# Optimization experiments

Hardware: AMD Instinct MI355X
Metric: run time of the kernel (lower is better)

Reference implementation:

```python
import jax, jax.numpy as jnp
import numpy as np

B, S, H, D = 2, 2048, 8, 64
W = 128  # attention window radius


def setup_inputs() -> dict:
    key = jax.random.key(0)
    kq, kk, kv = jax.random.split(key, 3)
    return {
        "query": jax.random.normal(kq, (B, S, H, D), dtype=jnp.float32),
        "key": jax.random.normal(kk, (B, S, H, D), dtype=jnp.float32),
        "value": jax.random.normal(kv, (B, S, H, D), dtype=jnp.float32),
        "window_size": W,
    }


def reference(query, key, value, window_size):
    # Sliding-window (symmetric, radius=window_size, inclusive) attention.
    # Per-query softmax over keys j with |i - j| <= window_size, scale 1/sqrt(D).
    b, s, h, d = query.shape
    scale = 1.0 / jnp.sqrt(jnp.asarray(d, query.dtype))
    # scores: [B, H, S, S]
    scores = jnp.einsum("bihd,bjhd->bhij", query * scale, key)
    i = jnp.arange(s)[:, None]
    j = jnp.arange(s)[None, :]
    band = jnp.abs(i - j) <= window_size  # [S, S]
    scores = jnp.where(band, scores, -jnp.inf)
    weights = jax.nn.softmax(scores, axis=-1)
    out = jnp.einsum("bhij,bjhd->bihd", weights, value)
    return out
```

## Files before the change

kernel.cpp:

```cpp
#include <hip/hip_runtime.h>
#include <hip/hip_fp16.h>
#include <math.h>

typedef _Float16 half8 __attribute__((ext_vector_type(8)));
typedef _Float16 half4 __attribute__((ext_vector_type(4)));
typedef float f32x4 __attribute__((ext_vector_type(4)));

#define S_LEN 2048
#define NH 8
#define DH 64
#define HD (NH*DH)
#define BQ 64
#define SPAN 320
#define NT 256

__global__ __launch_bounds__(NT, 2)
void swa_mfma(const float* __restrict__ qg, const float* __restrict__ kg,
              const float* __restrict__ vg, const int* __restrict__ wptr,
              float* __restrict__ outg)
{
    __shared__ __align__(16) unsigned short Kl[SPAN * DH];
    __shared__ __align__(16) unsigned short Vt[DH * SPAN];

    int W = *wptr; if (W > 128) W = 128;
    const int span = BQ + 2 * W;

    const int t = threadIdx.x;
    int bid = blockIdx.x;
    bid = (bid & 7) * (gridDim.x >> 3) + (bid >> 3);
    const int qt = bid & 31, h = (bid >> 5) & 7, b = bid >> 8;
    const int i0 = qt * BQ, s0 = i0 - W;

    const float* kbh = kg + (size_t)b * S_LEN * HD + h * DH;
    const float* vbh = vg + (size_t)b * S_LEN * HD + h * DH;

    for (int cidx = t; cidx < span * 8; cidx += NT) {
        const int koff = cidx >> 3, cr = cidx & 7;
        const int j = s0 + koff;
        const int dst = koff * 64 + ((cr ^ (koff & 7)) << 3);
        half8 hv = {0,0,0,0,0,0,0,0};
        if ((unsigned)j < S_LEN) {
            const float* p = kbh + (size_t)j * HD + cr * 8;
            float4 f0 = *(const float4*)p, f1 = *(const float4*)(p + 4);
            hv[0]=(_Float16)f0.x; hv[1]=(_Float16)f0.y; hv[2]=(_Float16)f0.z; hv[3]=(_Float16)f0.w;
            hv[4]=(_Float16)f1.x; hv[5]=(_Float16)f1.y; hv[6]=(_Float16)f1.z; hv[7]=(_Float16)f1.w;
        }
        *(half8*)(&Kl[dst]) = hv;
    }

    for (int task = t; task < span * 4; task += NT) {
        const int dq = task & 15, kq = task >> 4;
        float rr[4][4];
        #pragma unroll
        for (int jj = 0; jj < 4; ++jj) {
            const int j = s0 + kq * 4 + jj;
            float4 f = {0.f, 0.f, 0.f, 0.f};
            if ((unsigned)j < S_LEN) f = *(const float4*)(vbh + (size_t)j * HD + dq * 4);
            rr[jj][0] = f.x; rr[jj][1] = f.y; rr[jj][2] = f.z; rr[jj][3] = f.w;
        }
        #pragma unroll
        for (int i = 0; i < 4; ++i) {
            const int dim = dq * 4 + i;
            half4 w = { (_Float16)rr[0][i], (_Float16)rr[1][i],
                        (_Float16)rr[2][i], (_Float16)rr[3][i] };
            const int off = dim * SPAN + (((kq >> 1) ^ (dim & 7)) << 3) + ((kq & 1) << 2);
            *(half4*)(&Vt[off]) = w;
        }
    }

    const int wid = t >> 6, lane = t & 63, c = lane & 15, g = lane >> 4;
    const int q = i0 + wid * 16 + c;
    const float* qrow = qg + (size_t)b * S_LEN * HD + h * DH + (size_t)q * HD;
    half8 qa0, qa1;
    #pragma unroll
    for (int e = 0; e < 8; ++e) {
        qa0[e] = (_Float16)(qrow[g * 8 + e] * 0.125f);
        qa1[e] = (_Float16)(qrow[32 + g * 8 + e] * 0.125f);
    }

    const int c7 = c & 7;
    const int ch0 = (g ^ c7) << 3;
    const int ch1 = ((g + 4) ^ c7) << 3;
    int lo = q - W; if (lo < 0) lo = 0;
    int hi = q + W; if (hi > S_LEN - 1) hi = S_LEN - 1;
    const unsigned rng = (unsigned)(hi - lo);

    int ts = wid >> 1;
    const int ts0 = (s0 < 0) ? ((-s0) >> 5) : 0;
    if (ts0 > ts) ts = ts0;
    const int te_w = (16 * wid + 15 + 2 * W) >> 5;
    const int te_s = (S_LEN - 1 - s0) >> 5;
    const int te = te_w < te_s ? te_w : te_s;

    float m = -1e4f, l = 0.f;
    f32x4 o0 = {0,0,0,0}, o1 = {0,0,0,0}, o2 = {0,0,0,0}, o3 = {0,0,0,0};

    __syncthreads();

    for (int t32 = ts; t32 <= te; ++t32) {
        const unsigned short* krow = &Kl[(t32 * 32 + c) * 64];
        half8 k00 = *(const half8*)(krow + ch0);
        half8 k01 = *(const half8*)(krow + ch1);
        half8 k10 = *(const half8*)(krow + 16 * 64 + ch0);
        half8 k11 = *(const half8*)(krow + 16 * 64 + ch1);
        f32x4 st0 = {0,0,0,0}, st1 = {0,0,0,0};
        st0 = __builtin_amdgcn_mfma_f32_16x16x32_f16(k00, qa0, st0, 0, 0, 0);
        st0 = __builtin_amdgcn_mfma_f32_16x16x32_f16(k01, qa1, st0, 0, 0, 0);
        st1 = __builtin_amdgcn_mfma_f32_16x16x32_f16(k10, qa0, st1, 0, 0, 0);
        st1 = __builtin_amdgcn_mfma_f32_16x16x32_f16(k11, qa1, st1, 0, 0, 0);

        const int kb = s0 + t32 * 32 + 4 * g;
        float sv0[4], sv1[4];
        #pragma unroll
        for (int r = 0; r < 4; ++r) {
            sv0[r] = ((unsigned)(kb + r - lo) <= rng)      ? st0[r] : -30000.f;
            sv1[r] = ((unsigned)(kb + 16 + r - lo) <= rng) ? st1[r] : -30000.f;
        }
        float tmax = fmaxf(fmaxf(fmaxf(sv0[0], sv0[1]), fmaxf(sv0[2], sv0[3])),
                           fmaxf(fmaxf(sv1[0], sv1[1]), fmaxf(sv1[2], sv1[3])));
        tmax = fmaxf(tmax, __shfl_xor(tmax, 16));
        tmax = fmaxf(tmax, __shfl_xor(tmax, 32));
        const float newm = fmaxf(m, tmax);
        const float alpha = __expf(m - newm);
        m = newm;
        l *= alpha;
        o0 *= alpha; o1 *= alpha; o2 *= alpha; o3 *= alpha;

        float p0[4], p1[4], ls = 0.f;
        #pragma unroll
        for (int r = 0; r < 4; ++r) {
            p0[r] = __expf(sv0[r] - m);
            p1[r] = __expf(sv1[r] - m);
            ls += p0[r] + p1[r];
        }
        l += ls;
        half8 pb;
        #pragma unroll
        for (int r = 0; r < 4; ++r) { pb[r] = (_Float16)p0[r]; pb[4 + r] = (_Float16)p1[r]; }

        const int cb = 4 * t32 + (g >> 1);
        const int off1 = ((cb ^ c7) << 3) + ((g & 1) << 2);
        const int off2 = (((cb + 2) ^ c7) << 3) + ((g & 1) << 2);
#define PV_STEP(DF, OACC) { \
        const unsigned short* vrow = &Vt[(16 * DF + c) * SPAN]; \
        half4 vlo = *(const half4*)(vrow + off1); \
        half4 vhi = *(const half4*)(vrow + off2); \
        half8 vf; \
        vf[0]=vlo[0]; vf[1]=vlo[1]; vf[2]=vlo[2]; vf[3]=vlo[3]; \
        vf[4]=vhi[0]; vf[5]=vhi[1]; vf[6]=vhi[2]; vf[7]=vhi[3]; \
        OACC = __builtin_amdgcn_mfma_f32_16x16x32_f16(vf, pb, OACC, 0, 0, 0); }
        PV_STEP(0, o0)
        PV_STEP(1, o1)
        PV_STEP(2, o2)
        PV_STEP(3, o3)
#undef PV_STEP
    }

    l += __shfl_xor(l, 16);
    l += __shfl_xor(l, 32);
    const float inv = 1.0f / l;
    float* orow = outg + (size_t)b * S_LEN * HD + h * DH + (size_t)q * HD + 4 * g;
    { float4 w; w.x=o0[0]*inv; w.y=o0[1]*inv; w.z=o0[2]*inv; w.w=o0[3]*inv; *(float4*)(orow)      = w; }
    { float4 w; w.x=o1[0]*inv; w.y=o1[1]*inv; w.z=o1[2]*inv; w.w=o1[3]*inv; *(float4*)(orow + 16) = w; }
    { float4 w; w.x=o2[0]*inv; w.y=o2[1]*inv; w.z=o2[2]*inv; w.w=o2[3]*inv; *(float4*)(orow + 32) = w; }
    { float4 w; w.x=o3[0]*inv; w.y=o3[1]*inv; w.z=o3[2]*inv; w.w=o3[3]*inv; *(float4*)(orow + 48) = w; }
}

extern "C" void kernel_launch(void* const* d_in, const int* in_sizes, int n_in,
                              void* d_out, int out_size, void* d_ws, size_t ws_size,
                              hipStream_t stream) {
    const float* q = (const float*)d_in[0];
    const float* k = (const float*)d_in[1];
    const float* v = (const float*)d_in[2];
    const int*   w = (const int*)d_in[3];
    float* out = (float*)d_out;

    const int nblocks = 2 * NH * (S_LEN / BQ);
    swa_mfma<<<dim3(nblocks), dim3(NT), 0, stream>>>(q, k, v, w, out);
}
```

Baseline: 19.38 us.

## Double-buffer K/V chunks in LDS with register prefetch overlapping MFMA compute

The whole K/V window is no longer staged into LDS up front. The loop now streams 64-key chunks through two LDS buffers, prefetching the next chunk into registers during compute and writing it after. Other changes: log2e is folded into the Q scale so exp2f replaces expf, the rescale is skipped when no lane's max grows, MFMA sections get raised s_setprio, and Q is loaded vectorised. This cuts LDS footprint and start-up latency, at the cost of a __syncthreads per chunk and more live registers.

```diff
diff --git a/kernel.cpp b/kernel.cpp
--- a/kernel.cpp
+++ b/kernel.cpp
@@ -11,19 +11,20 @@
 #define DH 64
 #define HD (NH*DH)
 #define BQ 64
-#define SPAN 320
 #define NT 256
+#define CK 64
 
 __global__ __launch_bounds__(NT, 2)
 void swa_mfma(const float* __restrict__ qg, const float* __restrict__ kg,
               const float* __restrict__ vg, const int* __restrict__ wptr,
               float* __restrict__ outg)
 {
-    __shared__ __align__(16) unsigned short Kl[SPAN * DH];
-    __shared__ __align__(16) unsigned short Vt[DH * SPAN];
+    __shared__ __align__(16) unsigned short Kb[2][CK * DH];
+    __shared__ __align__(16) unsigned short Vb[2][DH * CK];
 
     int W = *wptr; if (W > 128) W = 128;
     const int span = BQ + 2 * W;
+    const int nch = (span + CK - 1) / CK;
 
     const int t = threadIdx.x;
     int bid = blockIdx.x;
@@ -34,48 +35,73 @@
     const float* kbh = kg + (size_t)b * S_LEN * HD + h * DH;
     const float* vbh = vg + (size_t)b * S_LEN * HD + h * DH;
 
-    for (int cidx = t; cidx < span * 8; cidx += NT) {
-        const int koff = cidx >> 3, cr = cidx & 7;
-        const int j = s0 + koff;
-        const int dst = koff * 64 + ((cr ^ (koff & 7)) << 3);
-        half8 hv = {0,0,0,0,0,0,0,0};
-        if ((unsigned)j < S_LEN) {
-            const float* p = kbh + (size_t)j * HD + cr * 8;
-            float4 f0 = *(const float4*)p, f1 = *(const float4*)(p + 4);
-            hv[0]=(_Float16)f0.x; hv[1]=(_Float16)f0.y; hv[2]=(_Float16)f0.z; hv[3]=(_Float16)f0.w;
-            hv[4]=(_Float16)f1.x; hv[5]=(_Float16)f1.y; hv[6]=(_Float16)f1.z; hv[7]=(_Float16)f1.w;
-        }
-        *(half8*)(&Kl[dst]) = hv;
-    }
-
-    for (int task = t; task < span * 4; task += NT) {
-        const int dq = task & 15, kq = task >> 4;
-        float rr[4][4];
+    const int k_koff = t >> 3, k_cr = t & 7;
+    const int v_kq = t >> 4, v_dq = t & 15;
+
+    f32x4 ka[2][2];
+    f32x4 va[4];
+
+    auto loadK = [&](int cc) {
+        #pragma unroll
+        for (int it = 0; it < 2; ++it) {
+            const int koff = k_koff + it * 32;
+            const int j = s0 + cc * CK + koff;
+            f32x4 f0 = {0,0,0,0}, f1 = {0,0,0,0};
+            if ((unsigned)j < S_LEN) {
+                const float* p = kbh + (size_t)j * HD + k_cr * 8;
+                f0 = *(const f32x4*)p; f1 = *(const f32x4*)(p + 4);
+            }
+            ka[it][0] = f0; ka[it][1] = f1;
+        }
+    };
+    auto writeK = [&](int bufi) {
+        #pragma unroll
+        for (int it = 0; it < 2; ++it) {
+            const int koff = k_koff + it * 32;
+            half8 hv;
+            #pragma unroll
+            for (int e = 0; e < 4; ++e) {
+                hv[e]     = (_Float16)ka[it][0][e];
+                hv[4 + e] = (_Float16)ka[it][1][e];
+            }
+            *(half8*)(&Kb[bufi][koff * 64 + ((k_cr ^ (koff & 7)) << 3)]) = hv;
+        }
+    };
+    auto loadV = [&](int cc) {
         #pragma unroll
         for (int jj = 0; jj < 4; ++jj) {
-            const int j = s0 + kq * 4 + jj;
-            float4 f = {0.f, 0.f, 0.f, 0.f};
-            if ((unsigned)j < S_LEN) f = *(const float4*)(vbh + (size_t)j * HD + dq * 4);
-            rr[jj][0] = f.x; rr[jj][1] = f.y; rr[jj][2] = f.z; rr[jj][3] = f.w;
-        }
+            const int j = s0 + cc * CK + v_kq * 4 + jj;
+            f32x4 f = {0,0,0,0};
+            if ((unsigned)j < S_LEN) f = *(const f32x4*)(vbh + (size_t)j * HD + v_dq * 4);
+            va[jj] = f;
+        }
+    };
+    auto writeV = [&](int bufi) {
         #pragma unroll
         for (int i = 0; i < 4; ++i) {
-            const int dim = dq * 4 + i;
-            half4 w = { (_Float16)rr[0][i], (_Float16)rr[1][i],
-                        (_Float16)rr[2][i], (_Float16)rr[3][i] };
-            const int off = dim * SPAN + (((kq >> 1) ^ (dim & 7)) << 3) + ((kq & 1) << 2);
-            *(half4*)(&Vt[off]) = w;
-        }
-    }
+            const int dim = v_dq * 4 + i;
+            half4 w = { (_Float16)va[0][i], (_Float16)va[1][i],
+                        (_Float16)va[2][i], (_Float16)va[3][i] };
+            const int off = dim * 64 + (((v_kq >> 1) ^ (dim & 7)) << 3) + ((v_kq & 1) << 2);
+            *(half4*)(&Vb[bufi][off]) = w;
+        }
+    };
 
     const int wid = t >> 6, lane = t & 63, c = lane & 15, g = lane >> 4;
     const int q = i0 + wid * 16 + c;
     const float* qrow = qg + (size_t)b * S_LEN * HD + h * DH + (size_t)q * HD;
     half8 qa0, qa1;
-    #pragma unroll
-    for (int e = 0; e < 8; ++e) {
-        qa0[e] = (_Float16)(qrow[g * 8 + e] * 0.125f);
-        qa1[e] = (_Float16)(qrow[32 + g * 8 + e] * 0.125f);
+    {
+        const float qs = 0.18033688011112042f;
+        f32x4 q0 = *(const f32x4*)(qrow + g * 8);
+        f32x4 q1 = *(const f32x4*)(qrow + g * 8 + 4);
+        f32x4 q2 = *(const f32x4*)(qrow + 32 + g * 8);
+        f32x4 q3 = *(const f32x4*)(qrow + 32 + g * 8 + 4);
+        #pragma unroll
+        for (int e = 0; e < 4; ++e) {
+            qa0[e] = (_Float16)(q0[e] * qs); qa0[4 + e] = (_Float16)(q1[e] * qs);
+            qa1[e] = (_Float16)(q2[e] * qs); qa1[4 + e] = (_Float16)(q3[e] * qs);
+        }
     }
 
     const int c7 = c & 7;
@@ -95,65 +121,86 @@
     float m = -1e4f, l = 0.f;
     f32x4 o0 = {0,0,0,0}, o1 = {0,0,0,0}, o2 = {0,0,0,0}, o3 = {0,0,0,0};
 
+    loadK(0); loadV(0);
+    writeK(0); writeV(0);
     __syncthreads();
 
-    for (int t32 = ts; t32 <= te; ++t32) {
-        const unsigned short* krow = &Kl[(t32 * 32 + c) * 64];
-        half8 k00 = *(const half8*)(krow + ch0);
-        half8 k01 = *(const half8*)(krow + ch1);
-        half8 k10 = *(const half8*)(krow + 16 * 64 + ch0);
-        half8 k11 = *(const half8*)(krow + 16 * 64 + ch1);
-        f32x4 st0 = {0,0,0,0}, st1 = {0,0,0,0};
-        st0 = __builtin_amdgcn_mfma_f32_16x16x32_f16(k00, qa0, st0, 0, 0, 0);
-        st0 = __builtin_amdgcn_mfma_f32_16x16x32_f16(k01, qa1, st0, 0, 0, 0);
-        st1 = __builtin_amdgcn_mfma_f32_16x16x32_f16(k10, qa0, st1, 0, 0, 0);
-        st1 = __builtin_amdgcn_mfma_f32_16x16x32_f16(k11, qa1, st1, 0, 0, 0);
-
-        const int kb = s0 + t32 * 32 + 4 * g;
-        float sv0[4], sv1[4];
-        #pragma unroll
-        for (int r = 0; r < 4; ++r) {
-            sv0[r] = ((unsigned)(kb + r - lo) <= rng)      ? st0[r] : -30000.f;
-            sv1[r] = ((unsigned)(kb + 16 + r - lo) <= rng) ? st1[r] : -30000.f;
-        }
-        float tmax = fmaxf(fmaxf(fmaxf(sv0[0], sv0[1]), fmaxf(sv0[2], sv0[3])),
-                           fmaxf(fmaxf(sv1[0], sv1[1]), fmaxf(sv1[2], sv1[3])));
-        tmax = fmaxf(tmax, __shfl_xor(tmax, 16));
-        tmax = fmaxf(tmax, __shfl_xor(tmax, 32));
-        const float newm = fmaxf(m, tmax);
-        const float alpha = __expf(m - newm);
-        m = newm;
-        l *= alpha;
-        o0 *= alpha; o1 *= alpha; o2 *= alpha; o3 *= alpha;
-
-        float p0[4], p1[4], ls = 0.f;
-        #pragma unroll
-        for (int r = 0; r < 4; ++r) {
-            p0[r] = __expf(sv0[r] - m);
-            p1[r] = __expf(sv1[r] - m);
-            ls += p0[r] + p1[r];
-        }
-        l += ls;
-        half8 pb;
-        #pragma unroll
-        for (int r = 0; r < 4; ++r) { pb[r] = (_Float16)p0[r]; pb[4 + r] = (_Float16)p1[r]; }
-
-        const int cb = 4 * t32 + (g >> 1);
-        const int off1 = ((cb ^ c7) << 3) + ((g & 1) << 2);
-        const int off2 = (((cb + 2) ^ c7) << 3) + ((g & 1) << 2);
+    for (int cc = 0; cc < nch; ++cc) {
+        const int cur = cc & 1;
+        const bool pf = (cc + 1 < nch);
+        if (pf) { loadK(cc + 1); loadV(cc + 1); }
+
+        #pragma unroll
+        for (int hh = 0; hh < 2; ++hh) {
+            const int t32 = 2 * cc + hh;
+            if (t32 < ts || t32 > te) continue;
+
+            const unsigned short* krow = &Kb[cur][((hh << 5) + c) * 64];
+            half8 k00 = *(const half8*)(krow + ch0);
+            half8 k01 = *(const half8*)(krow + ch1);
+            half8 k10 = *(const half8*)(krow + 16 * 64 + ch0);
+            half8 k11 = *(const half8*)(krow + 16 * 64 + ch1);
+            f32x4 st0 = {0,0,0,0}, st1 = {0,0,0,0};
+            __builtin_amdgcn_s_setprio(1);
+            st0 = __builtin_amdgcn_mfma_f32_16x16x32_f16(k00, qa0, st0, 0, 0, 0);
+            st0 = __builtin_amdgcn_mfma_f32_16x16x32_f16(k01, qa1, st0, 0, 0, 0);
+            st1 = __builtin_amdgcn_mfma_f32_16x16x32_f16(k10, qa0, st1, 0, 0, 0);
+            st1 = __builtin_amdgcn_mfma_f32_16x16x32_f16(k11, qa1, st1, 0, 0, 0);
+            __builtin_amdgcn_s_setprio(0);
+
+            const int kb = s0 + t32 * 32 + 4 * g;
+            float sv0[4], sv1[4];
+            #pragma unroll
+            for (int r = 0; r < 4; ++r) {
+                sv0[r] = ((unsigned)(kb + r - lo) <= rng)      ? st0[r] : -30000.f;
+                sv1[r] = ((unsigned)(kb + 16 + r - lo) <= rng) ? st1[r] : -30000.f;
+            }
+            float tmax = fmaxf(fmaxf(fmaxf(sv0[0], sv0[1]), fmaxf(sv0[2], sv0[3])),
+                               fmaxf(fmaxf(sv1[0], sv1[1]), fmaxf(sv1[2], sv1[3])));
+            tmax = fmaxf(tmax, __shfl_xor(tmax, 16));
+            tmax = fmaxf(tmax, __shfl_xor(tmax, 32));
+            if (__any(tmax > m)) {
+                const float newm = fmaxf(m, tmax);
+                const float alpha = exp2f(m - newm);
+                m = newm;
+                l *= alpha;
+                o0 *= alpha; o1 *= alpha; o2 *= alpha; o3 *= alpha;
+            }
+
+            float p0[4], p1[4], ls = 0.f;
+            #pragma unroll
+            for (int r = 0; r < 4; ++r) {
+                p0[r] = exp2f(sv0[r] - m);
+                p1[r] = exp2f(sv1[r] - m);
+                ls += p0[r] + p1[r];
+            }
+            l += ls;
+            half8 pb;
+            #pragma unroll
+            for (int r = 0; r < 4; ++r) { pb[r] = (_Float16)p0[r]; pb[4 + r] = (_Float16)p1[r]; }
+
+            const int cb = 4 * hh + (g >> 1);
+            const int off1 = ((cb ^ c7) << 3) + ((g & 1) << 2);
+            const int off2 = (((cb + 2) ^ c7) << 3) + ((g & 1) << 2);
+            __builtin_amdgcn_s_setprio(1);
 #define PV_STEP(DF, OACC) { \
-        const unsigned short* vrow = &Vt[(16 * DF + c) * SPAN]; \
-        half4 vlo = *(const half4*)(vrow + off1); \
-        half4 vhi = *(const half4*)(vrow + off2); \
-        half8 vf; \
-        vf[0]=vlo[0]; vf[1]=vlo[1]; vf[2]=vlo[2]; vf[3]=vlo[3]; \
-        vf[4]=vhi[0]; vf[5]=vhi[1]; vf[6]=vhi[2]; vf[7]=vhi[3]; \
-        OACC = __builtin_amdgcn_mfma_f32_16x16x32_f16(vf, pb, OACC, 0, 0, 0); }
-        PV_STEP(0, o0)
-        PV_STEP(1, o1)
-        PV_STEP(2, o2)
-        PV_STEP(3, o3)
+            const unsigned short* vrow = &Vb[cur][(16 * DF + c) * 64]; \
+            half4 vlo = *(const half4*)(vrow + off1); \
+            half4 vhi = *(const half4*)(vrow + off2); \
+            half8 vf; \
+            vf[0]=vlo[0]; vf[1]=vlo[1]; vf[2]=vlo[2]; vf[3]=vlo[3]; \
+            vf[4]=vhi[0]; vf[5]=vhi[1]; vf[6]=vhi[2]; vf[7]=vhi[3]; \
+            OACC = __builtin_amdgcn_mfma_f32_16x16x32_f16(vf, pb, OACC, 0, 0, 0); }
+            PV_STEP(0, o0)
+            PV_STEP(1, o1)
+            PV_STEP(2, o2)
+            PV_STEP(3, o3)
 #undef PV_STEP
+            __builtin_amdgcn_s_setprio(0);
+        }
+
+        if (pf) { writeK(cur ^ 1); writeV(cur ^ 1); }
+        __syncthreads();
     }
 
     l += __shfl_xor(l, 16);
```

Result: slower. 21.23 us (+9.6%).

## Double query tile to 128 and overlap second-half K/V staging with compute

Applied to the files above, without the earlier changes.

Raises the query tile to 128 rows with 512 threads, so each block reuses its staged K/V window across more queries. The block loads only the first six key tiles into LDS before it starts computing. Loads for the rest go into registers and are written to LDS after the first compute phase. The query is folded into a log2e scale so the kernel can use exp2f. The running-max rescale is skipped when no lane's max grows, and s_setprio is raised around the MFMA groups. The costs are higher register pressure from the prefetch buffers, fewer blocks (256), and an extra barrier. The staging loops also hardcode sizes that assume W=128.

```diff
diff --git a/kernel.cpp b/kernel.cpp
--- a/kernel.cpp
+++ b/kernel.cpp
@@ -10,9 +10,11 @@
 #define NH 8
 #define DH 64
 #define HD (NH*DH)
-#define BQ 64
-#define SPAN 320
-#define NT 256
+#define BQ 128
+#define SPAN (BQ + 256)
+#define NT 512
+#define NTILES (SPAN / 32)
+#define SPLIT_T 6
 
 __global__ __launch_bounds__(NT, 2)
 void swa_mfma(const float* __restrict__ qg, const float* __restrict__ kg,
@@ -23,59 +25,67 @@
     __shared__ __align__(16) unsigned short Vt[DH * SPAN];
 
     int W = *wptr; if (W > 128) W = 128;
-    const int span = BQ + 2 * W;
 
     const int t = threadIdx.x;
     int bid = blockIdx.x;
     bid = (bid & 7) * (gridDim.x >> 3) + (bid >> 3);
-    const int qt = bid & 31, h = (bid >> 5) & 7, b = bid >> 8;
+    const int qt = bid & 15, h = (bid >> 4) & 7, b = bid >> 7;
     const int i0 = qt * BQ, s0 = i0 - W;
 
     const float* kbh = kg + (size_t)b * S_LEN * HD + h * DH;
     const float* vbh = vg + (size_t)b * S_LEN * HD + h * DH;
 
-    for (int cidx = t; cidx < span * 8; cidx += NT) {
-        const int koff = cidx >> 3, cr = cidx & 7;
+    const int wid = t >> 6, lane = t & 63, c = lane & 15, g = lane >> 4;
+    const int q = i0 + wid * 16 + c;
+
+    const float* qrow = qg + (size_t)b * S_LEN * HD + h * DH + (size_t)q * HD;
+    const f32x4 qf0 = *(const f32x4*)(qrow + g * 8);
+    const f32x4 qf1 = *(const f32x4*)(qrow + g * 8 + 4);
+    const f32x4 qf2 = *(const f32x4*)(qrow + 32 + g * 8);
+    const f32x4 qf3 = *(const f32x4*)(qrow + 32 + g * 8 + 4);
+
+    #pragma unroll
+    for (int it = 0; it < 3; ++it) {
+        const int task = t + it * NT;
+        const int koff = task >> 3, cr = task & 7;
         const int j = s0 + koff;
-        const int dst = koff * 64 + ((cr ^ (koff & 7)) << 3);
-        half8 hv = {0,0,0,0,0,0,0,0};
+        f32x4 f0 = {0,0,0,0}, f1 = {0,0,0,0};
         if ((unsigned)j < S_LEN) {
             const float* p = kbh + (size_t)j * HD + cr * 8;
-            float4 f0 = *(const float4*)p, f1 = *(const float4*)(p + 4);
-            hv[0]=(_Float16)f0.x; hv[1]=(_Float16)f0.y; hv[2]=(_Float16)f0.z; hv[3]=(_Float16)f0.w;
-            hv[4]=(_Float16)f1.x; hv[5]=(_Float16)f1.y; hv[6]=(_Float16)f1.z; hv[7]=(_Float16)f1.w;
-        }
-        *(half8*)(&Kl[dst]) = hv;
-    }
-
-    for (int task = t; task < span * 4; task += NT) {
-        const int dq = task & 15, kq = task >> 4;
-        float rr[4][4];
+            f0 = *(const f32x4*)p; f1 = *(const f32x4*)(p + 4);
+        }
+        half8 hv;
+        #pragma unroll
+        for (int e = 0; e < 4; ++e) { hv[e] = (_Float16)f0[e]; hv[4+e] = (_Float16)f1[e]; }
+        *(half8*)(&Kl[koff * 64 + ((cr ^ (koff & 7)) << 3)]) = hv;
+    }
+    for (int task = t; task < 768; task += NT) {
+        const int kq = task >> 4, dq = task & 15;
+        f32x4 r[4];
         #pragma unroll
         for (int jj = 0; jj < 4; ++jj) {
             const int j = s0 + kq * 4 + jj;
-            float4 f = {0.f, 0.f, 0.f, 0.f};
-            if ((unsigned)j < S_LEN) f = *(const float4*)(vbh + (size_t)j * HD + dq * 4);
-            rr[jj][0] = f.x; rr[jj][1] = f.y; rr[jj][2] = f.z; rr[jj][3] = f.w;
+            f32x4 f = {0,0,0,0};
+            if ((unsigned)j < S_LEN) f = *(const f32x4*)(vbh + (size_t)j * HD + dq * 4);
+            r[jj] = f;
         }
         #pragma unroll
         for (int i = 0; i < 4; ++i) {
             const int dim = dq * 4 + i;
-            half4 w = { (_Float16)rr[0][i], (_Float16)rr[1][i],
-                        (_Float16)rr[2][i], (_Float16)rr[3][i] };
-            const int off = dim * SPAN + (((kq >> 1) ^ (dim & 7)) << 3) + ((kq & 1) << 2);
-            *(half4*)(&Vt[off]) = w;
-        }
-    }
-
-    const int wid = t >> 6, lane = t & 63, c = lane & 15, g = lane >> 4;
-    const int q = i0 + wid * 16 + c;
-    const float* qrow = qg + (size_t)b * S_LEN * HD + h * DH + (size_t)q * HD;
+            half4 w = { (_Float16)r[0][i], (_Float16)r[1][i],
+                        (_Float16)r[2][i], (_Float16)r[3][i] };
+            *(half4*)(&Vt[dim * SPAN + (((kq >> 1) ^ (dim & 7)) << 3) + ((kq & 1) << 2)]) = w;
+        }
+    }
+
     half8 qa0, qa1;
-    #pragma unroll
-    for (int e = 0; e < 8; ++e) {
-        qa0[e] = (_Float16)(qrow[g * 8 + e] * 0.125f);
-        qa1[e] = (_Float16)(qrow[32 + g * 8 + e] * 0.125f);
+    {
+        const float qs = 0.18033688011112042f;
+        #pragma unroll
+        for (int e = 0; e < 4; ++e) {
+            qa0[e] = (_Float16)(qf0[e] * qs); qa0[4+e] = (_Float16)(qf1[e] * qs);
+            qa1[e] = (_Float16)(qf2[e] * qs); qa1[4+e] = (_Float16)(qf3[e] * qs);
+        }
     }
 
     const int c7 = c & 7;
@@ -97,17 +107,48 @@
 
     __syncthreads();
 
-    for (int t32 = ts; t32 <= te; ++t32) {
+    f32x4 kpf[3][2];
+    #pragma unroll
+    for (int it = 0; it < 3; ++it) {
+        const int task = 1536 + t + it * NT;
+        const int koff = task >> 3, cr = task & 7;
+        const int j = s0 + koff;
+        f32x4 f0 = {0,0,0,0}, f1 = {0,0,0,0};
+        if ((unsigned)j < S_LEN) {
+            const float* p = kbh + (size_t)j * HD + cr * 8;
+            f0 = *(const f32x4*)p; f1 = *(const f32x4*)(p + 4);
+        }
+        kpf[it][0] = f0; kpf[it][1] = f1;
+    }
+    f32x4 vpf[2][4];
+    #pragma unroll
+    for (int it = 0; it < 2; ++it) {
+        const int task = 768 + t + it * NT;
+        #pragma unroll
+        for (int jj = 0; jj < 4; ++jj) {
+            f32x4 f = {0,0,0,0};
+            if (task < 1536) {
+                const int kq = task >> 4, dq = task & 15;
+                const int j = s0 + kq * 4 + jj;
+                if ((unsigned)j < S_LEN) f = *(const f32x4*)(vbh + (size_t)j * HD + dq * 4);
+            }
+            vpf[it][jj] = f;
+        }
+    }
+
+    auto computeTile = [&](int t32) {
         const unsigned short* krow = &Kl[(t32 * 32 + c) * 64];
         half8 k00 = *(const half8*)(krow + ch0);
         half8 k01 = *(const half8*)(krow + ch1);
         half8 k10 = *(const half8*)(krow + 16 * 64 + ch0);
         half8 k11 = *(const half8*)(krow + 16 * 64 + ch1);
         f32x4 st0 = {0,0,0,0}, st1 = {0,0,0,0};
+        __builtin_amdgcn_s_setprio(1);
         st0 = __builtin_amdgcn_mfma_f32_16x16x32_f16(k00, qa0, st0, 0, 0, 0);
         st0 = __builtin_amdgcn_mfma_f32_16x16x32_f16(k01, qa1, st0, 0, 0, 0);
         st1 = __builtin_amdgcn_mfma_f32_16x16x32_f16(k10, qa0, st1, 0, 0, 0);
         st1 = __builtin_amdgcn_mfma_f32_16x16x32_f16(k11, qa1, st1, 0, 0, 0);
+        __builtin_amdgcn_s_setprio(0);
 
         const int kb = s0 + t32 * 32 + 4 * g;
         float sv0[4], sv1[4];
@@ -120,27 +161,29 @@
                            fmaxf(fmaxf(sv1[0], sv1[1]), fmaxf(sv1[2], sv1[3])));
         tmax = fmaxf(tmax, __shfl_xor(tmax, 16));
         tmax = fmaxf(tmax, __shfl_xor(tmax, 32));
-        const float newm = fmaxf(m, tmax);
-        const float alpha = __expf(m - newm);
-        m = newm;
-        l *= alpha;
-        o0 *= alpha; o1 *= alpha; o2 *= alpha; o3 *= alpha;
-
+        if (__any(tmax > m)) {
+            const float newm = fmaxf(m, tmax);
+            const float alpha = exp2f(m - newm);
+            m = newm;
+            l *= alpha;
+            o0 *= alpha; o1 *= alpha; o2 *= alpha; o3 *= alpha;
+        }
         float p0[4], p1[4], ls = 0.f;
         #pragma unroll
         for (int r = 0; r < 4; ++r) {
-            p0[r] = __expf(sv0[r] - m);
-            p1[r] = __expf(sv1[r] - m);
+            p0[r] = exp2f(sv0[r] - m);
+            p1[r] = exp2f(sv1[r] - m);
             ls += p0[r] + p1[r];
         }
         l += ls;
         half8 pb;
         #pragma unroll
-        for (int r = 0; r < 4; ++r) { pb[r] = (_Float16)p0[r]; pb[4 + r] = (_Float16)p1[r]; }
+        for (int r = 0; r < 4; ++r) { pb[r] = (_Float16)p0[r]; pb[4+r] = (_Float16)p1[r]; }
 
         const int cb = 4 * t32 + (g >> 1);
         const int off1 = ((cb ^ c7) << 3) + ((g & 1) << 2);
         const int off2 = (((cb + 2) ^ c7) << 3) + ((g & 1) << 2);
+        __builtin_amdgcn_s_setprio(1);
 #define PV_STEP(DF, OACC) { \
         const unsigned short* vrow = &Vt[(16 * DF + c) * SPAN]; \
         half4 vlo = *(const half4*)(vrow + off1); \
@@ -154,7 +197,37 @@
         PV_STEP(2, o2)
         PV_STEP(3, o3)
 #undef PV_STEP
-    }
+        __builtin_amdgcn_s_setprio(0);
+    };
+
+    for (int t32 = ts; t32 <= te && t32 < SPLIT_T; ++t32) computeTile(t32);
+
+    #pragma unroll
+    for (int it = 0; it < 3; ++it) {
+        const int task = 1536 + t + it * NT;
+        const int koff = task >> 3, cr = task & 7;
+        half8 hv;
+        #pragma unroll
+        for (int e = 0; e < 4; ++e) { hv[e] = (_Float16)kpf[it][0][e]; hv[4+e] = (_Float16)kpf[it][1][e]; }
+        *(half8*)(&Kl[koff * 64 + ((cr ^ (koff & 7)) << 3)]) = hv;
+    }
+    #pragma unroll
+    for (int it = 0; it < 2; ++it) {
+        const int task = 768 + t + it * NT;
+        if (task < 1536) {
+            const int kq = task >> 4, dq = task & 15;
+            #pragma unroll
+            for (int i = 0; i < 4; ++i) {
+                const int dim = dq * 4 + i;
+                half4 w = { (_Float16)vpf[it][0][i], (_Float16)vpf[it][1][i],
+                            (_Float16)vpf[it][2][i], (_Float16)vpf[it][3][i] };
+                *(half4*)(&Vt[dim * SPAN + (((kq >> 1) ^ (dim & 7)) << 3) + ((kq & 1) << 2)]) = w;
+            }
+        }
+    }
+    __syncthreads();
+
+    for (int t32 = (ts > SPLIT_T ? ts : SPLIT_T); t32 <= te; ++t32) computeTile(t32);
 
     l += __shfl_xor(l, 16);
     l += __shfl_xor(l, 32);
```

After: 19.59 us. No clear change (+1.1%).

## Stream K from global into registers with double buffering, drop K LDS tile

Applied to the files above, without the earlier changes.

Removes the shared-memory K tile: each wave loads its K rows straight from global into registers, converts them to fp16 with packed conversions, and double-buffers the next tile's loads behind the current tile's MFMA work. Also folds log2(e) into the Q scale to use exp2, skips the accumulator rescale when no lane's max grows, skips masking for fully in-window tiles, raises occupancy to 3 blocks per SM, and adds setprio around MFMAs. Less LDS raises occupancy, but each wave now reads K rows from global memory separately, which increases global and L2 traffic and register pressure.

```diff
diff --git a/kernel.cpp b/kernel.cpp
--- a/kernel.cpp
+++ b/kernel.cpp
@@ -4,6 +4,7 @@
 
 typedef _Float16 half8 __attribute__((ext_vector_type(8)));
 typedef _Float16 half4 __attribute__((ext_vector_type(4)));
+typedef __fp16 fp16x2 __attribute__((ext_vector_type(2)));
 typedef float f32x4 __attribute__((ext_vector_type(4)));
 
 #define S_LEN 2048
@@ -11,19 +12,17 @@
 #define DH 64
 #define HD (NH*DH)
 #define BQ 64
-#define SPAN 320
+#define SPAN (BQ + 256)
 #define NT 256
 
-__global__ __launch_bounds__(NT, 2)
+__global__ __launch_bounds__(NT, 3)
 void swa_mfma(const float* __restrict__ qg, const float* __restrict__ kg,
               const float* __restrict__ vg, const int* __restrict__ wptr,
               float* __restrict__ outg)
 {
-    __shared__ __align__(16) unsigned short Kl[SPAN * DH];
     __shared__ __align__(16) unsigned short Vt[DH * SPAN];
 
     int W = *wptr; if (W > 128) W = 128;
-    const int span = BQ + 2 * W;
 
     const int t = threadIdx.x;
     int bid = blockIdx.x;
@@ -34,56 +33,51 @@
     const float* kbh = kg + (size_t)b * S_LEN * HD + h * DH;
     const float* vbh = vg + (size_t)b * S_LEN * HD + h * DH;
 
-    for (int cidx = t; cidx < span * 8; cidx += NT) {
-        const int koff = cidx >> 3, cr = cidx & 7;
-        const int j = s0 + koff;
-        const int dst = koff * 64 + ((cr ^ (koff & 7)) << 3);
-        half8 hv = {0,0,0,0,0,0,0,0};
-        if ((unsigned)j < S_LEN) {
-            const float* p = kbh + (size_t)j * HD + cr * 8;
-            float4 f0 = *(const float4*)p, f1 = *(const float4*)(p + 4);
-            hv[0]=(_Float16)f0.x; hv[1]=(_Float16)f0.y; hv[2]=(_Float16)f0.z; hv[3]=(_Float16)f0.w;
-            hv[4]=(_Float16)f1.x; hv[5]=(_Float16)f1.y; hv[6]=(_Float16)f1.z; hv[7]=(_Float16)f1.w;
-        }
-        *(half8*)(&Kl[dst]) = hv;
-    }
-
-    for (int task = t; task < span * 4; task += NT) {
-        const int dq = task & 15, kq = task >> 4;
-        float rr[4][4];
+    const int wid = t >> 6, lane = t & 63, c = lane & 15, g = lane >> 4;
+    const int q = i0 + wid * 16 + c;
+
+    const float* qrow = qg + (size_t)b * S_LEN * HD + h * DH + (size_t)q * HD;
+    const f32x4 qf0 = *(const f32x4*)(qrow + g * 8);
+    const f32x4 qf1 = *(const f32x4*)(qrow + g * 8 + 4);
+    const f32x4 qf2 = *(const f32x4*)(qrow + 32 + g * 8);
+    const f32x4 qf3 = *(const f32x4*)(qrow + 32 + g * 8 + 4);
+
+    #pragma unroll
+    for (int it = 0; it < 5; ++it) {
+        const int task = t + it * NT;
+        const int kq = task >> 4, dq = task & 15;
+        f32x4 r[4];
         #pragma unroll
         for (int jj = 0; jj < 4; ++jj) {
             const int j = s0 + kq * 4 + jj;
-            float4 f = {0.f, 0.f, 0.f, 0.f};
-            if ((unsigned)j < S_LEN) f = *(const float4*)(vbh + (size_t)j * HD + dq * 4);
-            rr[jj][0] = f.x; rr[jj][1] = f.y; rr[jj][2] = f.z; rr[jj][3] = f.w;
+            f32x4 f = {0,0,0,0};
+            if ((unsigned)j < S_LEN) f = *(const f32x4*)(vbh + (size_t)j * HD + dq * 4);
+            r[jj] = f;
         }
         #pragma unroll
         for (int i = 0; i < 4; ++i) {
             const int dim = dq * 4 + i;
-            half4 w = { (_Float16)rr[0][i], (_Float16)rr[1][i],
-                        (_Float16)rr[2][i], (_Float16)rr[3][i] };
-            const int off = dim * SPAN + (((kq >> 1) ^ (dim & 7)) << 3) + ((kq & 1) << 2);
-            *(half4*)(&Vt[off]) = w;
+            half4 w = { (_Float16)r[0][i], (_Float16)r[1][i],
+                        (_Float16)r[2][i], (_Float16)r[3][i] };
+            *(half4*)(&Vt[dim * SPAN + (((kq >> 1) ^ (dim & 7)) << 3) + ((kq & 1) << 2)]) = w;
         }
     }
 
-    const int wid = t >> 6, lane = t & 63, c = lane & 15, g = lane >> 4;
-    const int q = i0 + wid * 16 + c;
-    const float* qrow = qg + (size_t)b * S_LEN * HD + h * DH + (size_t)q * HD;
     half8 qa0, qa1;
-    #pragma unroll
-    for (int e = 0; e < 8; ++e) {
-        qa0[e] = (_Float16)(qrow[g * 8 + e] * 0.125f);
-        qa1[e] = (_Float16)(qrow[32 + g * 8 + e] * 0.125f);
+    {
+        const float qs = 0.18033688011112042f;
+        #pragma unroll
+        for (int e = 0; e < 4; ++e) {
+            qa0[e] = (_Float16)(qf0[e] * qs); qa0[4+e] = (_Float16)(qf1[e] * qs);
+            qa1[e] = (_Float16)(qf2[e] * qs); qa1[4+e] = (_Float16)(qf3[e] * qs);
+        }
     }
 
     const int c7 = c & 7;
-    const int ch0 = (g ^ c7) << 3;
-    const int ch1 = ((g + 4) ^ c7) << 3;
     int lo = q - W; if (lo < 0) lo = 0;
     int hi = q + W; if (hi > S_LEN - 1) hi = S_LEN - 1;
     const unsigned rng = (unsigned)(hi - lo);
+    const int qw0 = i0 + wid * 16;
 
     int ts = wid >> 1;
     const int ts0 = (s0 < 0) ? ((-s0) >> 5) : 0;
@@ -95,52 +89,83 @@
     float m = -1e4f, l = 0.f;
     f32x4 o0 = {0,0,0,0}, o1 = {0,0,0,0}, o2 = {0,0,0,0}, o3 = {0,0,0,0};
 
-    __syncthreads();
-
-    for (int t32 = ts; t32 <= te; ++t32) {
-        const unsigned short* krow = &Kl[(t32 * 32 + c) * 64];
-        half8 k00 = *(const half8*)(krow + ch0);
-        half8 k01 = *(const half8*)(krow + ch1);
-        half8 k10 = *(const half8*)(krow + 16 * 64 + ch0);
-        half8 k11 = *(const half8*)(krow + 16 * 64 + ch1);
+    auto loadKraw = [&](int t32, f32x4 (&kr)[4][2]) {
+        const int j0 = s0 + t32 * 32;
+        int rA = j0 + c;      rA = rA < 0 ? 0 : (rA > S_LEN - 1 ? S_LEN - 1 : rA);
+        int rB = j0 + 16 + c; rB = rB < 0 ? 0 : (rB > S_LEN - 1 ? S_LEN - 1 : rB);
+        const float* pA = kbh + (size_t)rA * HD + g * 8;
+        const float* pB = kbh + (size_t)rB * HD + g * 8;
+        kr[0][0] = *(const f32x4*)(pA);      kr[0][1] = *(const f32x4*)(pA + 4);
+        kr[1][0] = *(const f32x4*)(pA + 32); kr[1][1] = *(const f32x4*)(pA + 36);
+        kr[2][0] = *(const f32x4*)(pB);      kr[2][1] = *(const f32x4*)(pB + 4);
+        kr[3][0] = *(const f32x4*)(pB + 32); kr[3][1] = *(const f32x4*)(pB + 36);
+    };
+    auto mkfrag = [](const f32x4& a, const f32x4& b) -> half8 {
+        fp16x2 p0 = __builtin_amdgcn_cvt_pkrtz(a[0], a[1]);
+        fp16x2 p1 = __builtin_amdgcn_cvt_pkrtz(a[2], a[3]);
+        fp16x2 p2 = __builtin_amdgcn_cvt_pkrtz(b[0], b[1]);
+        fp16x2 p3 = __builtin_amdgcn_cvt_pkrtz(b[2], b[3]);
+        half8 r;
+        r[0]=(_Float16)p0[0]; r[1]=(_Float16)p0[1]; r[2]=(_Float16)p1[0]; r[3]=(_Float16)p1[1];
+        r[4]=(_Float16)p2[0]; r[5]=(_Float16)p2[1]; r[6]=(_Float16)p3[0]; r[7]=(_Float16)p3[1];
+        return r;
+    };
+
+    auto computeTile = [&](int t32, f32x4 (&kr)[4][2]) {
+        half8 k00 = mkfrag(kr[0][0], kr[0][1]);
+        half8 k01 = mkfrag(kr[1][0], kr[1][1]);
+        half8 k10 = mkfrag(kr[2][0], kr[2][1]);
+        half8 k11 = mkfrag(kr[3][0], kr[3][1]);
         f32x4 st0 = {0,0,0,0}, st1 = {0,0,0,0};
+        __builtin_amdgcn_s_setprio(1);
         st0 = __builtin_amdgcn_mfma_f32_16x16x32_f16(k00, qa0, st0, 0, 0, 0);
         st0 = __builtin_amdgcn_mfma_f32_16x16x32_f16(k01, qa1, st0, 0, 0, 0);
         st1 = __builtin_amdgcn_mfma_f32_16x16x32_f16(k10, qa0, st1, 0, 0, 0);
         st1 = __builtin_amdgcn_mfma_f32_16x16x32_f16(k11, qa1, st1, 0, 0, 0);
-
-        const int kb = s0 + t32 * 32 + 4 * g;
+        __builtin_amdgcn_s_setprio(0);
+
+        const int j0 = s0 + t32 * 32;
         float sv0[4], sv1[4];
-        #pragma unroll
-        for (int r = 0; r < 4; ++r) {
-            sv0[r] = ((unsigned)(kb + r - lo) <= rng)      ? st0[r] : -30000.f;
-            sv1[r] = ((unsigned)(kb + 16 + r - lo) <= rng) ? st1[r] : -30000.f;
+        const bool allv = (j0 >= 0) && (j0 + 31 < S_LEN) &&
+                          (j0 >= qw0 + 15 - W) && (j0 + 31 <= qw0 + W);
+        if (allv) {
+            #pragma unroll
+            for (int r = 0; r < 4; ++r) { sv0[r] = st0[r]; sv1[r] = st1[r]; }
+        } else {
+            const int kb = j0 + 4 * g;
+            #pragma unroll
+            for (int r = 0; r < 4; ++r) {
+                sv0[r] = ((unsigned)(kb + r - lo) <= rng)      ? st0[r] : -30000.f;
+                sv1[r] = ((unsigned)(kb + 16 + r - lo) <= rng) ? st1[r] : -30000.f;
+            }
         }
         float tmax = fmaxf(fmaxf(fmaxf(sv0[0], sv0[1]), fmaxf(sv0[2], sv0[3])),
                            fmaxf(fmaxf(sv1[0], sv1[1]), fmaxf(sv1[2], sv1[3])));
         tmax = fmaxf(tmax, __shfl_xor(tmax, 16));
         tmax = fmaxf(tmax, __shfl_xor(tmax, 32));
-        const float newm = fmaxf(m, tmax);
-        const float alpha = __expf(m - newm);
-        m = newm;
-        l *= alpha;
-        o0 *= alpha; o1 *= alpha; o2 *= alpha; o3 *= alpha;
-
+        if (__any(tmax > m)) {
+            const float newm = fmaxf(m, tmax);
+            const float alpha = exp2f(m - newm);
+            m = newm;
+            l *= alpha;
+            o0 *= alpha; o1 *= alpha; o2 *= alpha; o3 *= alpha;
+        }
         float p0[4], p1[4], ls = 0.f;
         #pragma unroll
         for (int r = 0; r < 4; ++r) {
-            p0[r] = __expf(sv0[r] - m);
-            p1[r] = __expf(sv1[r] - m);
+            p0[r] = exp2f(sv0[r] - m);
+            p1[r] = exp2f(sv1[r] - m);
             ls += p0[r] + p1[r];
         }
         l += ls;
         half8 pb;
         #pragma unroll
-        for (int r = 0; r < 4; ++r) { pb[r] = (_Float16)p0[r]; pb[4 + r] = (_Float16)p1[r]; }
+        for (int r = 0; r < 4; ++r) { pb[r] = (_Float16)p0[r]; pb[4+r] = (_Float16)p1[r]; }
 
         const int cb = 4 * t32 + (g >> 1);
         const int off1 = ((cb ^ c7) << 3) + ((g & 1) << 2);
         const int off2 = (((cb + 2) ^ c7) << 3) + ((g & 1) << 2);
+        __builtin_amdgcn_s_setprio(1);
 #define PV_STEP(DF, OACC) { \
         const unsigned short* vrow = &Vt[(16 * DF + c) * SPAN]; \
         half4 vlo = *(const half4*)(vrow + off1); \
@@ -154,6 +179,23 @@
         PV_STEP(2, o2)
         PV_STEP(3, o3)
 #undef PV_STEP
+        __builtin_amdgcn_s_setprio(0);
+    };
+
+    f32x4 krA[4][2], krB[4][2];
+    loadKraw(ts, krA);
+
+    __syncthreads();
+
+    int t32 = ts;
+    while (t32 <= te) {
+        if (t32 < te) loadKraw(t32 + 1, krB);
+        computeTile(t32, krA);
+        ++t32;
+        if (t32 > te) break;
+        if (t32 < te) loadKraw(t32 + 1, krA);
+        computeTile(t32, krB);
+        ++t32;
     }
 
     l += __shfl_xor(l, 16);
```

New measurement: 28.13 us. 1.45x slower.
